# Kernel optimization log

Measured on AMD Instinct MI355X. Metric: run time of the kernel, lower is better.

## Reference

```python
import jax, jax.numpy as jnp
import numpy as np

EPS = 1e-5  # torch LayerNorm default


def setup_inputs() -> dict:
    key = jax.random.key(0)
    ks = jax.random.split(key, 7)
    B, s, i, c, h = 1, 1024, 512, 8, 8
    scale = 0.1
    return {
        "m": jax.random.normal(ks[0], (B, s, i, c), dtype=jnp.float32),
        "ln_gamma": jnp.ones((c,), dtype=jnp.float32),
        "ln_beta": jnp.zeros((c,), dtype=jnp.float32),
        "Wq": jax.random.normal(ks[1], (c * h, c), dtype=jnp.float32) * scale,
        "Wk": jax.random.normal(ks[2], (c, c), dtype=jnp.float32) * scale,
        "Wv": jax.random.normal(ks[3], (c, c), dtype=jnp.float32) * scale,
        "Wg": jax.random.normal(ks[4], (c * h, c), dtype=jnp.float32) * scale,
        "Wo": jax.random.normal(ks[5], (c, c * h), dtype=jnp.float32) * scale,
        "bo": jnp.zeros((c,), dtype=jnp.float32),
    }


def reference(m, ln_gamma, ln_beta, Wq, Wk, Wv, Wg, Wo, bo):
    c = Wk.shape[0]
    h = Wq.shape[0] // c
    B, s, i, _ = m.shape

    # LayerNorm over the channel dim c
    mu = jnp.mean(m, axis=-1, keepdims=True)
    var = jnp.mean(jnp.square(m - mu), axis=-1, keepdims=True)
    x = (m - mu) * jax.lax.rsqrt(var + EPS) * ln_gamma + ln_beta  # (B,s,i,c)

    # projections (torch Linear: y = x @ W.T)
    q = (x @ Wq.T).reshape(B, s, i, h, c).mean(axis=1)            # (B,i,h,c) mean-pooled query
    k = x @ Wk.T                                                   # (B,s,i,c)
    v = x @ Wv.T                                                   # (B,s,i,c)
    gate = jax.nn.sigmoid(x @ Wg.T).reshape(B, s, i, h, c)        # (B,s,i,h,c)

    # attention logits over the column axis t (=s), softmax along t (dim=-3 of b t i h)
    a = jnp.einsum('bihc,btic->btih', q, k) * (c ** -0.5)          # (B,s,i,h)
    a = jax.nn.softmax(a, axis=1)

    o = gate * jnp.einsum('btih,btic->btihc', a, v)               # (B,s,i,h,c)
    o = o.reshape(B, s, i, h * c)
    return o @ Wo.T + bo                                           # (B,s,i,c)
```

## Files before the change

### kernel.cpp

```cpp
#include <hip/hip_runtime.h>

namespace {
constexpr int S = 1024, I = 512, C = 8, H = 8;
constexpr int R = 2;
constexpr float LNEPS = 1e-5f;
constexpr float SCALE = 0.35355339059327373f;
}

__device__ __forceinline__ float dot8(const float x[8], float4 a, float4 b) {
    float r = x[0] * a.x;
    r += x[1] * a.y; r += x[2] * a.z; r += x[3] * a.w;
    r += x[4] * b.x; r += x[5] * b.y; r += x[6] * b.z; r += x[7] * b.w;
    return r;
}

__device__ __forceinline__ void ln8(float4 a, float4 b, const float gm[8],
                                    const float bt[8], float x[8]) {
    x[0] = a.x; x[1] = a.y; x[2] = a.z; x[3] = a.w;
    x[4] = b.x; x[5] = b.y; x[6] = b.z; x[7] = b.w;
    float mu = 0.f;
#pragma unroll
    for (int c = 0; c < 8; c++) mu += x[c];
    mu *= 0.125f;
    float var = 0.f;
#pragma unroll
    for (int c = 0; c < 8; c++) { float d = x[c] - mu; var += d * d; }
    var *= 0.125f;
    float inv = rsqrtf(var + LNEPS);
#pragma unroll
    for (int c = 0; c < 8; c++) x[c] = (x[c] - mu) * inv * gm[c] + bt[c];
}

__global__ __launch_bounds__(1024) void fused(
    const float* __restrict__ m, const float* __restrict__ gamma,
    const float* __restrict__ beta, const float* __restrict__ Wq,
    const float* __restrict__ Wk, const float* __restrict__ Wv,
    const float* __restrict__ Wg, const float* __restrict__ Wo,
    const float* __restrict__ bo, float* __restrict__ out) {
    __shared__ __align__(16) float sWoT[512];
    __shared__ __align__(16) float swred[16 * 16];
    __shared__ __align__(16) float sxbar[16];
    __shared__ __align__(16) float sqk[128];
    __shared__ __align__(16) float srden[16];

    int t = threadIdx.x;
    int w = t >> 6;
    int col = t & 1;
    int si = t >> 1;
    int i = 2 * blockIdx.x + col;

    if (t < 512) {
        int j = t & 63, c2 = t >> 6;
        sWoT[j * 8 + c2] = Wo[c2 * 64 + j];
    }

    float gm[8], bt[8];
#pragma unroll
    for (int c = 0; c < 8; c++) { gm[c] = gamma[c]; bt[c] = beta[c]; }

    const float4* m4 = (const float4*)m;
    float x[R][8];
    float acc[8];
#pragma unroll
    for (int c = 0; c < 8; c++) acc[c] = 0.f;
#pragma unroll
    for (int r = 0; r < R; r++) {
        int row = (si + 512 * r) * I + i;
        ln8(m4[row * 2], m4[row * 2 + 1], gm, bt, x[r]);
#pragma unroll
        for (int c = 0; c < 8; c++) acc[c] += x[r][c];
    }
#pragma unroll
    for (int d = 2; d < 64; d <<= 1)
#pragma unroll
        for (int c = 0; c < 8; c++) acc[c] += __shfl_xor(acc[c], d, 64);
    if ((t & 63) < 2) {
#pragma unroll
        for (int c = 0; c < 8; c++) swred[w * 16 + col * 8 + c] = acc[c];
    }
    __syncthreads();
    if (t < 16) {
        float s = 0.f;
#pragma unroll
        for (int ww = 0; ww < 16; ww++) s += swred[ww * 16 + t];
        sxbar[t] = s;
    }
    __syncthreads();
    if (t < 128) {
        int qcol = t >> 6, h = (t >> 3) & 7, c2 = t & 7;
        float xb[8];
#pragma unroll
        for (int c3 = 0; c3 < 8; c3++) xb[c3] = sxbar[qcol * 8 + c3];
        float a = 0.f;
#pragma unroll
        for (int c = 0; c < 8; c++) {
            float qc = 0.f;
#pragma unroll
            for (int c3 = 0; c3 < 8; c3++)
                qc += xb[c3] * Wq[(h * 8 + c) * 8 + c3];
            a += qc * Wk[c * 8 + c2];
        }
        sqk[qcol * 64 + h * 8 + c2] = a * (SCALE / 1024.0f);
    }
    __syncthreads();

    const float4* sqk4 = (const float4*)sqk;
    {
        float e[8];
#pragma unroll
        for (int h = 0; h < 8; h++) {
            float4 q0 = sqk4[col * 16 + h * 2], q1 = sqk4[col * 16 + h * 2 + 1];
            float s = 0.f;
#pragma unroll
            for (int r = 0; r < R; r++) s += __expf(dot8(x[r], q0, q1));
            e[h] = s;
        }
#pragma unroll
        for (int d = 2; d < 64; d <<= 1)
#pragma unroll
            for (int h = 0; h < 8; h++) e[h] += __shfl_xor(e[h], d, 64);
        if ((t & 63) < 2) {
#pragma unroll
            for (int h = 0; h < 8; h++) swred[w * 16 + col * 8 + h] = e[h];
        }
    }
    __syncthreads();
    if (t < 16) {
        float s = 0.f;
#pragma unroll
        for (int ww = 0; ww < 16; ww++) s += swred[ww * 16 + t];
        srden[t] = 1.0f / s;
    }
    __syncthreads();

    const float4* Wv4 = (const float4*)Wv;
    const float4* Wg4 = (const float4*)Wg;
    const float4* sWoT4 = (const float4*)sWoT;

    float v[R][8];
#pragma unroll
    for (int c = 0; c < 8; c++) {
        float4 w0 = Wv4[c * 2], w1 = Wv4[c * 2 + 1];
#pragma unroll
        for (int r = 0; r < R; r++) v[r][c] = dot8(x[r], w0, w1);
    }

    float oacc[R][8];
#pragma unroll
    for (int r = 0; r < R; r++)
#pragma unroll
        for (int c2 = 0; c2 < 8; c2++) oacc[r][c2] = bo[c2];

#pragma unroll 1
    for (int h = 0; h < 8; h++) {
        float4 q0 = sqk4[col * 16 + h * 2], q1 = sqk4[col * 16 + h * 2 + 1];
        float rd = srden[col * 8 + h];
        float a_[R];
#pragma unroll
        for (int r = 0; r < R; r++)
            a_[r] = __expf(dot8(x[r], q0, q1)) * rd;
#pragma unroll
        for (int c = 0; c < 8; c++) {
            int hc = h * 8 + c;
            float4 wg0 = Wg4[hc * 2], wg1 = Wg4[hc * 2 + 1];
            float o_[R];
#pragma unroll
            for (int r = 0; r < R; r++) {
                float z = dot8(x[r], wg0, wg1);
                float gate = __builtin_amdgcn_rcpf(1.0f + __expf(-z));
                o_[r] = gate * a_[r] * v[r][c];
            }
            float4 wo0 = sWoT4[hc * 2], wo1 = sWoT4[hc * 2 + 1];
#pragma unroll
            for (int r = 0; r < R; r++) {
                oacc[r][0] += o_[r] * wo0.x; oacc[r][1] += o_[r] * wo0.y;
                oacc[r][2] += o_[r] * wo0.z; oacc[r][3] += o_[r] * wo0.w;
                oacc[r][4] += o_[r] * wo1.x; oacc[r][5] += o_[r] * wo1.y;
                oacc[r][6] += o_[r] * wo1.z; oacc[r][7] += o_[r] * wo1.w;
            }
        }
    }
    float4* out4 = (float4*)out;
#pragma unroll
    for (int r = 0; r < R; r++) {
        int row = (si + 512 * r) * I + i;
        out4[row * 2] = make_float4(oacc[r][0], oacc[r][1], oacc[r][2], oacc[r][3]);
        out4[row * 2 + 1] = make_float4(oacc[r][4], oacc[r][5], oacc[r][6], oacc[r][7]);
    }
}

extern "C" void kernel_launch(void* const* d_in, const int* in_sizes, int n_in,
                              void* d_out, int out_size, void* d_ws, size_t ws_size,
                              hipStream_t stream) {
    const float* m     = (const float*)d_in[0];
    const float* gamma = (const float*)d_in[1];
    const float* beta  = (const float*)d_in[2];
    const float* Wq    = (const float*)d_in[3];
    const float* Wk    = (const float*)d_in[4];
    const float* Wv    = (const float*)d_in[5];
    const float* Wg    = (const float*)d_in[6];
    const float* Wo    = (const float*)d_in[7];
    const float* bo    = (const float*)d_in[8];
    float* out = (float*)d_out;

    fused<<<I / 2, 1024, 0, stream>>>(m, gamma, beta, Wq, Wk, Wv, Wg, Wo, bo, out);
}
```

Before: 113.8 us.

## Split fused kernel into reduction pass and widely parallel output pass

Splits the single fused kernel into two launches. The first computes layernorm, the pooled query-key vectors and the softmax denominators, and writes them to workspace. The second launches 2048 blocks of 256 threads with one row per thread, recomputing layernorm and producing the gated output. This replaces the per-block serial heavy phase that ran on only 256 blocks with a much wider grid. The cost is a second kernel launch, a second read of m, and recomputing layernorm.

Result: slower. 124.1 us (+9.1%).

```diff
diff --git a/kernel.cpp b/kernel.cpp
--- a/kernel.cpp
+++ b/kernel.cpp
@@ -2,7 +2,6 @@
 
 namespace {
 constexpr int S = 1024, I = 512, C = 8, H = 8;
-constexpr int R = 2;
 constexpr float LNEPS = 1e-5f;
 constexpr float SCALE = 0.35355339059327373f;
 }
@@ -31,17 +30,14 @@
     for (int c = 0; c < 8; c++) x[c] = (x[c] - mu) * inv * gm[c] + bt[c];
 }
 
-__global__ __launch_bounds__(1024) void fused(
+__global__ __launch_bounds__(1024) void k_qkden(
     const float* __restrict__ m, const float* __restrict__ gamma,
     const float* __restrict__ beta, const float* __restrict__ Wq,
-    const float* __restrict__ Wk, const float* __restrict__ Wv,
-    const float* __restrict__ Wg, const float* __restrict__ Wo,
-    const float* __restrict__ bo, float* __restrict__ out) {
-    __shared__ __align__(16) float sWoT[512];
+    const float* __restrict__ Wk, float* __restrict__ qk_g,
+    float* __restrict__ rden_g) {
     __shared__ __align__(16) float swred[16 * 16];
     __shared__ __align__(16) float sxbar[16];
     __shared__ __align__(16) float sqk[128];
-    __shared__ __align__(16) float srden[16];
 
     int t = threadIdx.x;
     int w = t >> 6;
@@ -49,22 +45,17 @@
     int si = t >> 1;
     int i = 2 * blockIdx.x + col;
 
-    if (t < 512) {
-        int j = t & 63, c2 = t >> 6;
-        sWoT[j * 8 + c2] = Wo[c2 * 64 + j];
-    }
-
     float gm[8], bt[8];
 #pragma unroll
     for (int c = 0; c < 8; c++) { gm[c] = gamma[c]; bt[c] = beta[c]; }
 
     const float4* m4 = (const float4*)m;
-    float x[R][8];
+    float x[2][8];
     float acc[8];
 #pragma unroll
     for (int c = 0; c < 8; c++) acc[c] = 0.f;
 #pragma unroll
-    for (int r = 0; r < R; r++) {
+    for (int r = 0; r < 2; r++) {
         int row = (si + 512 * r) * I + i;
         ln8(m4[row * 2], m4[row * 2 + 1], gm, bt, x[r]);
 #pragma unroll
@@ -100,93 +91,116 @@
                 qc += xb[c3] * Wq[(h * 8 + c) * 8 + c3];
             a += qc * Wk[c * 8 + c2];
         }
-        sqk[qcol * 64 + h * 8 + c2] = a * (SCALE / 1024.0f);
+        float val = a * (SCALE / 1024.0f);
+        sqk[qcol * 64 + (t & 63)] = val;
+        qk_g[(2 * blockIdx.x + qcol) * 64 + (t & 63)] = val;
     }
     __syncthreads();
 
     const float4* sqk4 = (const float4*)sqk;
-    {
-        float e[8];
-#pragma unroll
-        for (int h = 0; h < 8; h++) {
-            float4 q0 = sqk4[col * 16 + h * 2], q1 = sqk4[col * 16 + h * 2 + 1];
-            float s = 0.f;
-#pragma unroll
-            for (int r = 0; r < R; r++) s += __expf(dot8(x[r], q0, q1));
-            e[h] = s;
-        }
-#pragma unroll
-        for (int d = 2; d < 64; d <<= 1)
-#pragma unroll
-            for (int h = 0; h < 8; h++) e[h] += __shfl_xor(e[h], d, 64);
-        if ((t & 63) < 2) {
-#pragma unroll
-            for (int h = 0; h < 8; h++) swred[w * 16 + col * 8 + h] = e[h];
-        }
+    float e[8];
+#pragma unroll
+    for (int h = 0; h < 8; h++) {
+        float4 q0 = sqk4[col * 16 + h * 2], q1 = sqk4[col * 16 + h * 2 + 1];
+        float s = 0.f;
+#pragma unroll
+        for (int r = 0; r < 2; r++) s += __expf(dot8(x[r], q0, q1));
+        e[h] = s;
+    }
+#pragma unroll
+    for (int d = 2; d < 64; d <<= 1)
+#pragma unroll
+        for (int h = 0; h < 8; h++) e[h] += __shfl_xor(e[h], d, 64);
+    if ((t & 63) < 2) {
+#pragma unroll
+        for (int h = 0; h < 8; h++) swred[w * 16 + col * 8 + h] = e[h];
     }
     __syncthreads();
     if (t < 16) {
         float s = 0.f;
 #pragma unroll
         for (int ww = 0; ww < 16; ww++) s += swred[ww * 16 + t];
-        srden[t] = 1.0f / s;
-    }
-    __syncthreads();
+        rden_g[(2 * blockIdx.x + (t >> 3)) * 8 + (t & 7)] = 1.0f / s;
+    }
+}
+
+__global__ __launch_bounds__(256) void k_out(
+    const float* __restrict__ m, const float* __restrict__ gamma,
+    const float* __restrict__ beta, const float* __restrict__ Wv,
+    const float* __restrict__ Wg, const float* __restrict__ Wo,
+    const float* __restrict__ bo, const float* __restrict__ qk_g,
+    const float* __restrict__ rden_g, float* __restrict__ out) {
+    __shared__ __align__(16) float sWoT[512];
+    __shared__ __align__(16) float sqk[128];
+    __shared__ __align__(16) float srd[16];
+
+    int t = threadIdx.x;
+    int b = blockIdx.x;
+    int cp = b >> 3;
+    int rc = b & 7;
+    int col = t & 1;
+    int i = 2 * cp + col;
+    int s = rc * 128 + (t >> 1);
+
+#pragma unroll
+    for (int k = 0; k < 2; k++) {
+        int idx = t + 256 * k;
+        int j = idx & 63, c2 = idx >> 6;
+        sWoT[j * 8 + c2] = Wo[c2 * 64 + j];
+    }
+    if (t < 128) sqk[t] = qk_g[cp * 128 + t];
+    if (t < 16) srd[t] = rden_g[cp * 16 + t];
+    __syncthreads();
+
+    float gm[8], bt[8];
+#pragma unroll
+    for (int c = 0; c < 8; c++) { gm[c] = gamma[c]; bt[c] = beta[c]; }
+
+    const float4* m4 = (const float4*)m;
+    float x[8];
+    {
+        int row = s * I + i;
+        ln8(m4[row * 2], m4[row * 2 + 1], gm, bt, x);
+    }
 
     const float4* Wv4 = (const float4*)Wv;
+    float v[8];
+#pragma unroll
+    for (int c = 0; c < 8; c++) v[c] = dot8(x, Wv4[c * 2], Wv4[c * 2 + 1]);
+
+    const float4* sqk4 = (const float4*)sqk;
+    float p[8];
+#pragma unroll
+    for (int h = 0; h < 8; h++) {
+        float4 q0 = sqk4[col * 16 + h * 2], q1 = sqk4[col * 16 + h * 2 + 1];
+        p[h] = __expf(dot8(x, q0, q1)) * srd[col * 8 + h];
+    }
+
+    float oacc[8];
+#pragma unroll
+    for (int c2 = 0; c2 < 8; c2++) oacc[c2] = bo[c2];
+
     const float4* Wg4 = (const float4*)Wg;
     const float4* sWoT4 = (const float4*)sWoT;
-
-    float v[R][8];
-#pragma unroll
-    for (int c = 0; c < 8; c++) {
-        float4 w0 = Wv4[c * 2], w1 = Wv4[c * 2 + 1];
-#pragma unroll
-        for (int r = 0; r < R; r++) v[r][c] = dot8(x[r], w0, w1);
-    }
-
-    float oacc[R][8];
-#pragma unroll
-    for (int r = 0; r < R; r++)
-#pragma unroll
-        for (int c2 = 0; c2 < 8; c2++) oacc[r][c2] = bo[c2];
-
-#pragma unroll 1
+#pragma unroll
     for (int h = 0; h < 8; h++) {
-        float4 q0 = sqk4[col * 16 + h * 2], q1 = sqk4[col * 16 + h * 2 + 1];
-        float rd = srden[col * 8 + h];
-        float a_[R];
-#pragma unroll
-        for (int r = 0; r < R; r++)
-            a_[r] = __expf(dot8(x[r], q0, q1)) * rd;
 #pragma unroll
         for (int c = 0; c < 8; c++) {
             int hc = h * 8 + c;
-            float4 wg0 = Wg4[hc * 2], wg1 = Wg4[hc * 2 + 1];
-            float o_[R];
-#pragma unroll
-            for (int r = 0; r < R; r++) {
-                float z = dot8(x[r], wg0, wg1);
-                float gate = __builtin_amdgcn_rcpf(1.0f + __expf(-z));
-                o_[r] = gate * a_[r] * v[r][c];
-            }
+            float z = dot8(x, Wg4[hc * 2], Wg4[hc * 2 + 1]);
+            float gate = __builtin_amdgcn_rcpf(1.0f + __expf(-z));
+            float o_ = gate * p[h] * v[c];
             float4 wo0 = sWoT4[hc * 2], wo1 = sWoT4[hc * 2 + 1];
-#pragma unroll
-            for (int r = 0; r < R; r++) {
-                oacc[r][0] += o_[r] * wo0.x; oacc[r][1] += o_[r] * wo0.y;
-                oacc[r][2] += o_[r] * wo0.z; oacc[r][3] += o_[r] * wo0.w;
-                oacc[r][4] += o_[r] * wo1.x; oacc[r][5] += o_[r] * wo1.y;
-                oacc[r][6] += o_[r] * wo1.z; oacc[r][7] += o_[r] * wo1.w;
-            }
+            oacc[0] += o_ * wo0.x; oacc[1] += o_ * wo0.y;
+            oacc[2] += o_ * wo0.z; oacc[3] += o_ * wo0.w;
+            oacc[4] += o_ * wo1.x; oacc[5] += o_ * wo1.y;
+            oacc[6] += o_ * wo1.z; oacc[7] += o_ * wo1.w;
         }
     }
     float4* out4 = (float4*)out;
-#pragma unroll
-    for (int r = 0; r < R; r++) {
-        int row = (si + 512 * r) * I + i;
-        out4[row * 2] = make_float4(oacc[r][0], oacc[r][1], oacc[r][2], oacc[r][3]);
-        out4[row * 2 + 1] = make_float4(oacc[r][4], oacc[r][5], oacc[r][6], oacc[r][7]);
-    }
+    int row = s * I + i;
+    out4[row * 2] = make_float4(oacc[0], oacc[1], oacc[2], oacc[3]);
+    out4[row * 2 + 1] = make_float4(oacc[4], oacc[5], oacc[6], oacc[7]);
 }
 
 extern "C" void kernel_launch(void* const* d_in, const int* in_sizes, int n_in,
@@ -203,5 +217,11 @@
     const float* bo    = (const float*)d_in[8];
     float* out = (float*)d_out;
 
-    fused<<<I / 2, 1024, 0, stream>>>(m, gamma, beta, Wq, Wk, Wv, Wg, Wo, bo, out);
-}
+    float* ws     = (float*)d_ws;
+    float* qk_g   = ws;
+    float* rden_g = ws + (size_t)I * 64;
+
+    k_qkden<<<I / 2, 1024, 0, stream>>>(m, gamma, beta, Wq, Wk, qk_g, rden_g);
+    k_out<<<2048, 256, 0, stream>>>(m, gamma, beta, Wv, Wg, Wo, bo, qk_g,
+                                    rden_g, out);
+}
```
